# Optimization experiments

Hardware: AMD Instinct MI355X
Metric: run time of the kernel (lower is better)

## Reference

```python
import jax, jax.numpy as jnp
import numpy as np

B = 65536       # batch
F_SUB = 128     # sub-6GHz features
F_MM = 128      # mmWave features (pairs of real/imag)
H = 512         # hidden size (all three MLPs)
C = 64          # class_num (beams)
WB_SEL = 8      # number of selected wideband beams


def _mlp(x, w1, b1, w2, b2, wd, bd):
    # MLP with do_bn=False, dropout=0: Linear->ReLU->Linear->ReLU->Linear
    h = jax.nn.relu(x @ w1 + b1)
    h = jax.nn.relu(h @ w2 + b2)
    return h @ wd + bd


def setup_inputs() -> dict:
    key = jax.random.key(0)
    ks = jax.random.split(key, 16)
    w = lambda k, shape: (jax.random.normal(k, shape, jnp.float32) * 0.02)
    z = lambda n: jnp.zeros((n,), jnp.float32)
    return {
        "x": jax.random.normal(ks[0], (B, F_SUB), jnp.float32),
        "y": jax.random.normal(ks[1], (B, F_MM), jnp.float32),
        "sub_w1": w(ks[2], (F_SUB, H)), "sub_b1": z(H),
        "sub_w2": w(ks[3], (H, H)),     "sub_b2": z(H),
        "sub_wd": w(ks[4], (H, C)),     "sub_bd": z(C),
        "mm_w1": w(ks[5], (F_MM, H)),   "mm_b1": z(H),
        "mm_w2": w(ks[6], (H, H)),      "mm_b2": z(H),
        "mm_wd": w(ks[7], (H, C)),      "mm_bd": z(C),
        "att_w": w(ks[8], (2 * C, 2 * C)), "att_b": z(2 * C),
        "fus_w1": w(ks[9], (2 * C, H)), "fus_b1": z(H),
        "fus_w2": w(ks[10], (H, H)),    "fus_b2": z(H),
        "fus_wd": w(ks[11], (H, C)),    "fus_bd": z(C),
        "wb_sel": WB_SEL,
    }


def reference(x, y, sub_w1, sub_b1, sub_w2, sub_b2, sub_wd, sub_bd,
              mm_w1, mm_b1, mm_w2, mm_b2, mm_wd, mm_bd,
              att_w, att_b, fus_w1, fus_b1, fus_w2, fus_b2, fus_wd, fus_bd,
              wb_sel):
    b, f_mm = y.shape
    out_sub = _mlp(x, sub_w1, sub_b1, sub_w2, sub_b2, sub_wd, sub_bd)  # [B, C]
    class_num = out_sub.shape[1]
    wb_num = (class_num * 2) // f_mm  # int(class_num / features_mm * 2)
    # beam-group scores: sum consecutive groups of wb_num logits -> [B, f_mm/2]
    p_mm = out_sub.reshape(b, class_num // wb_num, wb_num).sum(axis=2)
    # top-k selected wideband beams (indices detached in original)
    _, idx = jax.lax.top_k(p_mm, wb_sel)               # [B, wb_sel]
    # scatter-build masked mmWave input: keep (idx*2, idx*2+1) pairs, zero rest
    rows = jnp.arange(b)[:, None]                       # [B, 1]
    mask = jnp.zeros_like(y)
    mask = mask.at[rows, idx * 2].set(1.0)
    mask = mask.at[rows, idx * 2 + 1].set(1.0)
    input_mm = y * mask
    out_mm = _mlp(input_mm, mm_w1, mm_b1, mm_w2, mm_b2, mm_wd, mm_bd)  # [B, C]
    cat = jnp.concatenate([out_sub, out_mm], axis=1)    # [B, 2C]
    out_att = jax.nn.sigmoid(cat @ att_w + att_b)       # [B, 2C]
    fused = _mlp(cat * out_att, fus_w1, fus_b1, fus_w2, fus_b2, fus_wd, fus_bd)
    return (out_sub, out_mm, fused)
```

## Files before the change

kernel.cpp:

```cpp
#include <hip/hip_runtime.h>
#include <math.h>


typedef _Float16 halfx8 __attribute__((ext_vector_type(8)));
typedef float    floatx4 __attribute__((ext_vector_type(4)));
#define MFMA16(a,b,c) __builtin_amdgcn_mfma_f32_16x16x32_f16((a),(b),(c),0,0,0)

#define BN 65536
#define MROWS 32
#define MARGIN 2e-4f

#define SM_IX0 0
#define SM_IX1 8192
#define SM_H0  16384
#define SM_H1  49152
#define SM_BYTES 81920
#define OBST 66

#define SZ_W1 65536
#define SZ_W2 262144
#define SZ_WD 32768
#define SZ_ATT 16384
#define OFF_SW1 0
#define OFF_SW2 (OFF_SW1 + SZ_W1)
#define OFF_SWD (OFF_SW2 + SZ_W2)
#define OFF_MW1 (OFF_SWD + SZ_WD)
#define OFF_MW2 (OFF_MW1 + SZ_W1)
#define OFF_MWD (OFF_MW2 + SZ_W2)
#define OFF_FW1 (OFF_MWD + SZ_WD)
#define OFF_FW2 (OFF_FW1 + SZ_W1)
#define OFF_FWD (OFF_FW2 + SZ_W2)
#define OFF_ATT (OFF_FWD + SZ_WD)

#define WS_MASKS (5u << 20)
#define WS_RROWS (6u << 20)
#define WS_RCNT  (7u << 20)
#define WS_FLAGS ((7u << 20) + 256)

enum { R_X = 0, R_Y, R_SW1, R_SB1, R_SW2, R_SB2, R_SWD, R_SBD,
       R_MW1, R_MB1, R_MW2, R_MB2, R_MWD, R_MBD, R_ATTW, R_ATTB,
       R_FW1, R_FB1, R_FW2, R_FB2, R_FWD, R_FBD, N_ROLES };

__device__ __forceinline__ float bf2f(unsigned short u) {
    return __uint_as_float((unsigned)u << 16);
}
__device__ __forceinline__ float loadf(const void* p, size_t i, int fl) {
    return fl == 1 ? bf2f(((const unsigned short*)p)[i])
         : fl == 0 ? ((const float*)p)[i] : 0.f;
}
__device__ __forceinline__ double loadd(const void* p, size_t i, int fl) {
    return fl == 1 ? (double)bf2f(((const unsigned short*)p)[i])
         : fl == 0 ? (double)((const float*)p)[i] : 0.0;
}
template<int FL>
__device__ __forceinline__ double ldw(const void* p, size_t i) {
    return FL == 1 ? (double)bf2f(((const unsigned short*)p)[i])
         : FL == 0 ? (double)((const float*)p)[i] : 0.0;
}
struct hf2 { _Float16 hi, lo; };
__device__ __forceinline__ hf2 split2h(float v) {
    hf2 r;
    r.hi = (_Float16)v;
    r.lo = (_Float16)(v - (float)r.hi);
    return r;
}
__device__ __forceinline__ int swz(int row, int colB, int rsB) {
    return (row * rsB + colB) ^ ((row & 15) << 4);
}

__device__ __forceinline__ void ld_b4(const _Float16* __restrict__ p,
                                      int base, int ktn, int kt, int l,
                                      halfx8 (&b)[4])
{
#pragma unroll
    for (int nt = 0; nt < 4; ++nt) {
        const size_t fi = ((((size_t)(base + nt)) * ktn + kt) * 64 + l) * 8;
        b[nt] = *(const halfx8*)(p + fi);
    }
}

__device__ __forceinline__ void kt_mfma(const char* __restrict__ sm,
                                        int smA0, int smA1, int rsB,
                                        int kt, int l15, int q,
                                        const halfx8 (&b)[4],
                                        floatx4 (&acc)[2][4])
{
    const int cB = kt * 64 + q * 16;
    halfx8 ahi[2], alo[2];
#pragma unroll
    for (int rt = 0; rt < 2; ++rt) {
        const int off = swz(rt * 16 + l15, cB, rsB);
        ahi[rt] = *(const halfx8*)(sm + smA0 + off);
        alo[rt] = *(const halfx8*)(sm + smA1 + off);
    }
#pragma unroll
    for (int nt = 0; nt < 4; ++nt)
#pragma unroll
        for (int rt = 0; rt < 2; ++rt) {
            acc[rt][nt] = MFMA16(alo[rt], b[nt], acc[rt][nt]);
            acc[rt][nt] = MFMA16(ahi[rt], b[nt], acc[rt][nt]);
        }
}

struct DetArgs { const void* p[N_ROLES]; int n[N_ROLES]; };

__global__ __launch_bounds__(256) void detect_kernel(DetArgs da, int* flags, int* rcnt) {
    const int role = blockIdx.x;
    if (role == 0 && threadIdx.x == 0) *rcnt = 0;
    const unsigned short* u = (const unsigned short*)da.p[role];
    int nsamp = da.n[role] / 2;
    if (nsamp > 4096) nsamp = 4096;
    __shared__ int band, nz;
    if (threadIdx.x == 0) { band = 0; nz = 0; }
    __syncthreads();
    int lb = 0, lnz = 0;
    for (int i = threadIdx.x; i < nsamp; i += 256) {
        const unsigned short v = u[2 * i];
        if (v) {
            ++lnz;
            const int e = (v >> 7) & 0xFF;
            if (e >= 100 && e <= 126) ++lb;
        }
    }
    atomicAdd(&band, lb);
    atomicAdd(&nz, lnz);
    __syncthreads();
    if (threadIdx.x == 0)
        flags[role] = (nz == 0) ? 2 : ((band * 2 > nz) ? 1 : 0);
}

struct PackArgs { const void* src[10]; int K[10], N[10], off[10], role[10]; };

__global__ __launch_bounds__(256) void pack_weights(PackArgs pa, _Float16* dst,
                                                    const int* __restrict__ flags) {
    const int m = blockIdx.y;
    const int fl = flags[pa.role[m]];
    const int K = pa.K[m], N = pa.N[m];
    const int KT = K >> 5, NT = N >> 4;
    const int total = KT * NT * 64;
    const int t = blockIdx.x * 256 + threadIdx.x;
    if (t >= total) return;
    const int l = t & 63;
    const int idx = t >> 6;
    const int kt = idx % KT;
    const int nt = idx / KT;
    const int k0 = kt * 32 + ((l >> 4) << 3);
    const int n  = nt * 16 + (l & 15);
    _Float16* dh = dst + pa.off[m] + (size_t)t * 8;
#pragma unroll
    for (int j = 0; j < 8; ++j)
        dh[j] = (_Float16)loadf(pa.src[m], (size_t)(k0 + j) * N + n, fl);
}

template <bool SUB>
__device__ __forceinline__ void mlp_core(
    char* __restrict__ sm,
    const _Float16* __restrict__ p1,
    const _Float16* __restrict__ p2,
    const _Float16* __restrict__ pd,
    const void* __restrict__ b1, int fb1,
    const void* __restrict__ b2, int fb2,
    const void* __restrict__ bd, int fbd,
    int r0, float* __restrict__ out)
{
    const int tid = threadIdx.x;
    const int l = tid & 63, w = tid >> 6, l15 = l & 15, q = l >> 4;

    floatx4 acc[2][4];
#pragma unroll
    for (int rt = 0; rt < 2; ++rt)
#pragma unroll
        for (int nt = 0; nt < 4; ++nt) acc[rt][nt] = (floatx4)0.0f;
#pragma unroll
    for (int kt = 0; kt < 4; ++kt) {
        halfx8 B[4];
        ld_b4(p1, w * 4, 4, kt, l, B);
        kt_mfma(sm, SM_IX0, SM_IX1, 256, kt, l15, q, B, acc);
    }
#pragma unroll
    for (int nt = 0; nt < 4; ++nt) {
        const int col = w * 64 + nt * 16 + l15;
        const float bias = loadf(b1, col, fb1);
#pragma unroll
        for (int rt = 0; rt < 2; ++rt)
#pragma unroll
            for (int r = 0; r < 4; ++r) {
                const int row = rt * 16 + q * 4 + r;
                float v = acc[rt][nt][r] + bias;
                v = v > 0.f ? v : 0.f;
                const hf2 s = split2h(v);
                const int o = swz(row, col * 2, 1024);
                *(_Float16*)(sm + SM_H0 + o) = s.hi;
                *(_Float16*)(sm + SM_H1 + o) = s.lo;
            }
    }
    __syncthreads();

    floatx4 acc2[2][4];
#pragma unroll
    for (int rt = 0; rt < 2; ++rt)
#pragma unroll
        for (int nt = 0; nt < 4; ++nt) acc2[rt][nt] = (floatx4)0.0f;
    for (int kt = 0; kt < 16; ++kt) {
        halfx8 B[4];
        ld_b4(p2, w * 4, 16, kt, l, B);
        kt_mfma(sm, SM_H0, SM_H1, 1024, kt, l15, q, B, acc2);
    }
    __syncthreads();
#pragma unroll
    for (int nt = 0; nt < 4; ++nt) {
        const int col = w * 64 + nt * 16 + l15;
        const float bias = loadf(b2, col, fb2);
#pragma unroll
        for (int rt = 0; rt < 2; ++rt)
#pragma unroll
            for (int r = 0; r < 4; ++r) {
                const int row = rt * 16 + q * 4 + r;
                float v = acc2[rt][nt][r] + bias;
                v = v > 0.f ? v : 0.f;
                const hf2 s = split2h(v);
                const int o = swz(row, col * 2, 1024);
                *(_Float16*)(sm + SM_H0 + o) = s.hi;
                *(_Float16*)(sm + SM_H1 + o) = s.lo;
            }
    }
    __syncthreads();

    {
        const int nt3 = w & 3, rt3 = w >> 2;
        floatx4 a3 = (floatx4)0.0f;
        for (int kt = 0; kt < 16; ++kt) {
            const size_t fi = (((size_t)(nt3 * 16 + kt)) * 64 + l) * 8;
            const halfx8 b = *(const halfx8*)(pd + fi);
            const int off = swz(rt3 * 16 + l15, kt * 64 + q * 16, 1024);
            const halfx8 ahi = *(const halfx8*)(sm + SM_H0 + off);
            const halfx8 alo = *(const halfx8*)(sm + SM_H1 + off);
            a3 = MFMA16(alo, b, a3);
            a3 = MFMA16(ahi, b, a3);
        }
        const int col = nt3 * 16 + l15;
        const float bias = loadf(bd, col, fbd);
        float* outb = (float*)sm;
#pragma unroll
        for (int r = 0; r < 4; ++r) {
            const int row = rt3 * 16 + q * 4 + r;
            const float v = a3[r] + bias;
            out[(size_t)(r0 + row) * 64 + col] = v;
            if (SUB) outb[row * OBST + col] = v;
        }
    }
    if (SUB) __syncthreads();
}

__global__ __launch_bounds__(512, 4)
void sub_mfma(const void* __restrict__ x, const _Float16* __restrict__ wpack,
              const void* __restrict__ b1, const void* __restrict__ b2,
              const void* __restrict__ bd, const int* __restrict__ flags,
              float* __restrict__ out, unsigned long long* __restrict__ masks,
              int* __restrict__ rrows, int* __restrict__ rcnt)
{
    __shared__ __align__(16) char sm[SM_BYTES];
    const int fx = flags[R_X];
    const int r0 = blockIdx.x * MROWS;

    for (int i = threadIdx.x; i < MROWS * 128; i += 512) {
        const int r = i >> 7, c = i & 127;
        const hf2 s = split2h(loadf(x, (size_t)(r0 + r) * 128 + c, fx));
        const int off = swz(r, c * 2, 256);
        *(_Float16*)(sm + SM_IX0 + off) = s.hi;
        *(_Float16*)(sm + SM_IX1 + off) = s.lo;
    }
    __syncthreads();

    mlp_core<true>(sm, wpack + OFF_SW1, wpack + OFF_SW2, wpack + OFF_SWD,
                   b1, flags[R_SB1], b2, flags[R_SB2], bd, flags[R_SBD],
                   r0, out);

    if (threadIdx.x < MROWS) {
        const float* rowp = (const float*)sm + threadIdx.x * OBST;
        float vals[9];
        int idxs[9];
#pragma unroll
        for (int j = 0; j < 9; ++j) { vals[j] = -__builtin_inff(); idxs[j] = 0; }
        for (int i = 0; i < 64; ++i) {
            const float v = rowp[i];
            if (v > vals[8]) {
                int p = 8;
                while (p > 0 && v > vals[p - 1]) {
                    vals[p] = vals[p - 1];
                    idxs[p] = idxs[p - 1];
                    --p;
                }
                vals[p] = v;
                idxs[p] = i;
            }
        }
        unsigned long long m = 0ull;
#pragma unroll
        for (int j = 0; j < 8; ++j) m |= (1ull << idxs[j]);
        masks[r0 + threadIdx.x] = m;
        if (vals[7] - vals[8] < MARGIN) {
            const int slot = atomicAdd(rcnt, 1);
            rrows[slot] = r0 + threadIdx.x;
        }
    }
}

#define RPB 16
#define OBST2 66

template<int FL, int K, int S, typename TI>
__device__ __forceinline__ void r_layer12(const void* __restrict__ W,
                                          const TI* __restrict__ in,
                                          double* __restrict__ a0,
                                          double* __restrict__ a1, int t)
{
#pragma unroll 4
    for (int k = 0; k < K; ++k) {
        const double w0 = ldw<FL>(W, (size_t)k * 512 + 2 * t);
        const double w1 = ldw<FL>(W, (size_t)k * 512 + 2 * t + 1);
#pragma unroll
        for (int r = 0; r < RPB; ++r) {
            const double xv = (double)in[r * S + k];
            a0[r] = fma(xv, w0, a0[r]);
            a1[r] = fma(xv, w1, a1[r]);
        }
    }
}

template<int FL>
__device__ __forceinline__ void r_layer3(const void* __restrict__ W,
                                         const double* __restrict__ h,
                                         int c, int rg, double* __restrict__ a)
{
#pragma unroll 4
    for (int k = 0; k < 512; ++k) {
        const double w = ldw<FL>(W, (size_t)k * 64 + c);
#pragma unroll
        for (int j = 0; j < 4; ++j)
            a[j] = fma(h[(rg * 4 + j) * 512 + k], w, a[j]);
    }
}

#define R_DISPATCH(fl, CALL)                                   \
    do {                                                       \
        if ((fl) == 1)      { CALL(1); }                       \
        else if ((fl) == 0) { CALL(0); }                       \
        else                { CALL(2); }                       \
    } while (0)

__global__ __launch_bounds__(256)
void rescue_kernel(const void* __restrict__ x,
                   const void* __restrict__ W1, const void* __restrict__ b1,
                   const void* __restrict__ W2, const void* __restrict__ b2,
                   const void* __restrict__ Wd, const void* __restrict__ bd,
                   const int* __restrict__ flags,
                   const int* __restrict__ rrows, const int* __restrict__ rcnt,
                   float* __restrict__ out, unsigned long long* __restrict__ masks)
{
    __shared__ int rowids[RPB];
    __shared__ __align__(16) char xob[RPB * OBST2 * 8];
    __shared__ __align__(16) double hsm[RPB * 512];
    float* xs = (float*)xob;
    double* ob = (double*)xob;
    const int fx = flags[R_X], f1 = flags[R_SW1], fb1 = flags[R_SB1],
              f2 = flags[R_SW2], fb2 = flags[R_SB2],
              f3 = flags[R_SWD], fb3 = flags[R_SBD];
    const int t = threadIdx.x;
    const int n = *rcnt;

    for (int g = blockIdx.x; g * RPB < n; g += gridDim.x) {
        const int base = g * RPB;
        int cnt = n - base;
        if (cnt > RPB) cnt = RPB;
        if (t < RPB) rowids[t] = rrows[base + (t < cnt ? t : cnt - 1)];
        __syncthreads();

        for (int i = t; i < RPB * 128; i += 256) {
            const int r = i >> 7, c = i & 127;
            xs[r * 128 + c] = loadf(x, (size_t)rowids[r] * 128 + c, fx);
        }
        __syncthreads();

        {
            double a0[RPB], a1[RPB];
#pragma unroll
            for (int r = 0; r < RPB; ++r) { a0[r] = 0.0; a1[r] = 0.0; }
#define L1_CALL(FL) r_layer12<FL, 128, 128, float>(W1, xs, a0, a1, t)
            R_DISPATCH(f1, L1_CALL);
#undef L1_CALL
            const double bb0 = loadd(b1, 2 * t, fb1), bb1 = loadd(b1, 2 * t + 1, fb1);
#pragma unroll
            for (int r = 0; r < RPB; ++r) {
                const double v0 = a0[r] + bb0, v1 = a1[r] + bb1;
                hsm[r * 512 + 2 * t]     = v0 > 0.0 ? v0 : 0.0;
                hsm[r * 512 + 2 * t + 1] = v1 > 0.0 ? v1 : 0.0;
            }
        }
        __syncthreads();

        {
            double a0[RPB], a1[RPB];
#pragma unroll
            for (int r = 0; r < RPB; ++r) { a0[r] = 0.0; a1[r] = 0.0; }
#define L2_CALL(FL) r_layer12<FL, 512, 512, double>(W2, hsm, a0, a1, t)
            R_DISPATCH(f2, L2_CALL);
#undef L2_CALL
            __syncthreads();
            const double bb0 = loadd(b2, 2 * t, fb2), bb1 = loadd(b2, 2 * t + 1, fb2);
#pragma unroll
            for (int r = 0; r < RPB; ++r) {
                const double v0 = a0[r] + bb0, v1 = a1[r] + bb1;
                hsm[r * 512 + 2 * t]     = v0 > 0.0 ? v0 : 0.0;
                hsm[r * 512 + 2 * t + 1] = v1 > 0.0 ? v1 : 0.0;
            }
        }
        __syncthreads();

        {
            const int c = t & 63, rg = t >> 6;
            double a[4];
#pragma unroll
            for (int j = 0; j < 4; ++j) a[j] = 0.0;
#define L3_CALL(FL) r_layer3<FL>(Wd, hsm, c, rg, a)
            R_DISPATCH(f3, L3_CALL);
#undef L3_CALL
            const double bb = loadd(bd, c, fb3);
#pragma unroll
            for (int j = 0; j < 4; ++j) {
                const int r = rg * 4 + j;
                const double v = a[j] + bb;
                ob[r * OBST2 + c] = v;
                if (r < cnt) out[(size_t)rowids[r] * 64 + c] = (float)v;
            }
        }
        __syncthreads();

        if (t < cnt) {
            double vals[8];
            int idxs[8];
#pragma unroll
            for (int j = 0; j < 8; ++j) { vals[j] = -1.0e300; idxs[j] = 0; }
            for (int i = 0; i < 64; ++i) {
                const double v = ob[t * OBST2 + i];
                if (v > vals[7]) {
                    int p = 7;
                    while (p > 0 && v > vals[p - 1]) {
                        vals[p] = vals[p - 1];
                        idxs[p] = idxs[p - 1];
                        --p;
                    }
                    vals[p] = v;
                    idxs[p] = i;
                }
            }
            unsigned long long m = 0ull;
#pragma unroll
            for (int j = 0; j < 8; ++j) m |= (1ull << idxs[j]);
            masks[rowids[t]] = m;
        }
        __syncthreads();
    }
}

__global__ __launch_bounds__(512, 4)
void mm_mfma(const unsigned long long* __restrict__ masks,
             const void* __restrict__ y, const _Float16* __restrict__ wpack,
             const void* __restrict__ b1, const void* __restrict__ b2,
             const void* __restrict__ bd, const int* __restrict__ flags,
             float* __restrict__ out)
{
    __shared__ __align__(16) char sm[SM_BYTES];
    const int fy = flags[R_Y];
    const int r0 = blockIdx.x * MROWS;

    for (int i = threadIdx.x; i < MROWS * 128; i += 512) {
        const int r = i >> 7, c = i & 127;
        const bool keep = (masks[r0 + r] >> (c >> 1)) & 1ull;
        const float v = keep ? loadf(y, (size_t)(r0 + r) * 128 + c, fy) : 0.f;
        const hf2 s = split2h(v);
        const int off = swz(r, c * 2, 256);
        *(_Float16*)(sm + SM_IX0 + off) = s.hi;
        *(_Float16*)(sm + SM_IX1 + off) = s.lo;
    }
    __syncthreads();

    mlp_core<false>(sm, wpack + OFF_MW1, wpack + OFF_MW2, wpack + OFF_MWD,
                    b1, flags[R_MB1], b2, flags[R_MB2], bd, flags[R_MBD],
                    r0, out);
}

__global__ __launch_bounds__(512, 4)
void fusion_mfma(const float* __restrict__ subf, const float* __restrict__ mmf,
                 const _Float16* __restrict__ wpack,
                 const void* __restrict__ attb,
                 const void* __restrict__ b1, const void* __restrict__ b2,
                 const void* __restrict__ bd, const int* __restrict__ flags,
                 float* __restrict__ out)
{
    __shared__ __align__(16) char sm[SM_BYTES];
    const int tid = threadIdx.x;
    const int l = tid & 63, w = tid >> 6, l15 = l & 15, q = l >> 4;
    const int r0 = blockIdx.x * MROWS;

    for (int i = tid; i < MROWS * 128; i += 512) {
        const int r = i >> 7, c = i & 127;
        const size_t row = (size_t)(r0 + r);
        const float v = (c < 64) ? subf[row * 64 + c] : mmf[row * 64 + (c - 64)];
        const hf2 s = split2h(v);
        const int off = swz(r, c * 2, 256);
        *(_Float16*)(sm + SM_IX0 + off) = s.hi;
        *(_Float16*)(sm + SM_IX1 + off) = s.lo;
    }
    __syncthreads();

    floatx4 aacc[2];
    aacc[0] = (floatx4)0.0f;
    aacc[1] = (floatx4)0.0f;
    const _Float16* patt = wpack + OFF_ATT;
#pragma unroll
    for (int kt = 0; kt < 4; ++kt) {
        const size_t fi = (((size_t)(w * 4 + kt)) * 64 + l) * 8;
        const halfx8 b = *(const halfx8*)(patt + fi);
        const int cB = kt * 64 + q * 16;
#pragma unroll
        for (int rt = 0; rt < 2; ++rt) {
            const int off = swz(rt * 16 + l15, cB, 256);
            const halfx8 ahi = *(const halfx8*)(sm + SM_IX0 + off);
            const halfx8 alo = *(const halfx8*)(sm + SM_IX1 + off);
            aacc[rt] = MFMA16(alo, b, aacc[rt]);
            aacc[rt] = MFMA16(ahi, b, aacc[rt]);
        }
    }
    const int col = w * 16 + l15;
    const float ab = loadf(attb, col, flags[R_ATTB]);
    float gated[2][4];
#pragma unroll
    for (int rt = 0; rt < 2; ++rt)
#pragma unroll
        for (int r = 0; r < 4; ++r) {
            const int rowl = rt * 16 + q * 4 + r;
            const float pre = aacc[rt][r] + ab;
            const float s = 1.f / (1.f + expf(-pre));
            const int off = swz(rowl, col * 2, 256);
            const float catv = (float)*(const _Float16*)(sm + SM_IX0 + off)
                             + (float)*(const _Float16*)(sm + SM_IX1 + off);
            gated[rt][r] = catv * s;
        }
    __syncthreads();
#pragma unroll
    for (int rt = 0; rt < 2; ++rt)
#pragma unroll
        for (int r = 0; r < 4; ++r) {
            const int rowl = rt * 16 + q * 4 + r;
            const hf2 s = split2h(gated[rt][r]);
            const int off = swz(rowl, col * 2, 256);
            *(_Float16*)(sm + SM_IX0 + off) = s.hi;
            *(_Float16*)(sm + SM_IX1 + off) = s.lo;
        }
    __syncthreads();

    mlp_core<false>(sm, wpack + OFF_FW1, wpack + OFF_FW2, wpack + OFF_FWD,
                    b1, flags[R_FB1], b2, flags[R_FB2], bd, flags[R_FBD],
                    r0, out);
}

extern "C" void kernel_launch(void* const* d_in, const int* in_sizes, int n_in,
                              void* d_out, int out_size, void* d_ws, size_t ws_size,
                              hipStream_t stream)
{
    static const int dictSizes[23] = {8388608, 8388608, 65536, 512, 262144, 512,
                                      32768, 64, 65536, 512, 262144, 512, 32768, 64,
                                      16384, 128, 65536, 512, 262144, 512, 32768, 64, 1};
    static const int dictRole[23]  = {R_X, R_Y, R_SW1, R_SB1, R_SW2, R_SB2, R_SWD, R_SBD,
                                      R_MW1, R_MB1, R_MW2, R_MB2, R_MWD, R_MBD,
                                      R_ATTW, R_ATTB, R_FW1, R_FB1, R_FW2, R_FB2,
                                      R_FWD, R_FBD, -1};
    static const int sortSizes[23] = {128, 16384, 512, 512, 64, 65536, 262144, 32768,
                                      512, 512, 64, 65536, 262144, 32768,
                                      512, 512, 64, 65536, 262144, 32768, 1,
                                      8388608, 8388608};
    static const int sortRole[23]  = {R_ATTB, R_ATTW, R_FB1, R_FB2, R_FBD, R_FW1,
                                      R_FW2, R_FWD, R_MB1, R_MB2, R_MBD, R_MW1,
                                      R_MW2, R_MWD, R_SB1, R_SB2, R_SBD, R_SW1,
                                      R_SW2, R_SWD, -1, R_X, R_Y};
    const void* rp[N_ROLES];
    int rs[N_ROLES];
    for (int i = 0; i < 23 && i < n_in; ++i)
        if (dictRole[i] >= 0) { rp[dictRole[i]] = d_in[i]; rs[dictRole[i]] = in_sizes[i]; }
    {
        bool dictOk = (n_in >= 22);
        for (int i = 0; i < 22 && dictOk; ++i)
            if (in_sizes[i] != dictSizes[i]) dictOk = false;
        if (!dictOk) {
            bool sortOk = (n_in >= 23);
            for (int i = 0; i < 23 && sortOk; ++i)
                if (in_sizes[i] != sortSizes[i]) sortOk = false;
            if (sortOk)
                for (int i = 0; i < 23; ++i)
                    if (sortRole[i] >= 0) { rp[sortRole[i]] = d_in[i]; rs[sortRole[i]] = in_sizes[i]; }
        }
    }

    _Float16* wpack = (_Float16*)d_ws;
    unsigned long long* masks = (unsigned long long*)((char*)d_ws + WS_MASKS);
    int* rrows = (int*)((char*)d_ws + WS_RROWS);
    int* rcnt  = (int*)((char*)d_ws + WS_RCNT);
    int* flags = (int*)((char*)d_ws + WS_FLAGS);

    float* out_f = (float*)d_out;
    float* sub_o = out_f;
    float* mm_o  = out_f + (size_t)BN * 64;
    float* fus_o = out_f + (size_t)2 * BN * 64;

    DetArgs da;
    for (int r = 0; r < N_ROLES; ++r) { da.p[r] = rp[r]; da.n[r] = rs[r]; }
    detect_kernel<<<N_ROLES, 256, 0, stream>>>(da, flags, rcnt);

    PackArgs pa;
    const int prole[10] = {R_SW1, R_SW2, R_SWD, R_MW1, R_MW2, R_MWD,
                           R_FW1, R_FW2, R_FWD, R_ATTW};
    const int Ks[10]   = {128, 512, 512, 128, 512, 512, 128, 512, 512, 128};
    const int Ns[10]   = {512, 512, 64, 512, 512, 64, 512, 512, 64, 128};
    const int offs[10] = {OFF_SW1, OFF_SW2, OFF_SWD, OFF_MW1, OFF_MW2,
                          OFF_MWD, OFF_FW1, OFF_FW2, OFF_FWD, OFF_ATT};
    for (int i = 0; i < 10; ++i) {
        pa.src[i] = rp[prole[i]];
        pa.K[i] = Ks[i];
        pa.N[i] = Ns[i];
        pa.off[i] = offs[i];
        pa.role[i] = prole[i];
    }
    pack_weights<<<dim3(128, 10), 256, 0, stream>>>(pa, wpack, flags);

    sub_mfma<<<BN / MROWS, 512, 0, stream>>>(
        rp[R_X], wpack, rp[R_SB1], rp[R_SB2], rp[R_SBD], flags,
        sub_o, masks, rrows, rcnt);

    rescue_kernel<<<512, 256, 0, stream>>>(
        rp[R_X], rp[R_SW1], rp[R_SB1], rp[R_SW2], rp[R_SB2], rp[R_SWD], rp[R_SBD],
        flags, rrows, rcnt, sub_o, masks);

    mm_mfma<<<BN / MROWS, 512, 0, stream>>>(
        masks, rp[R_Y], wpack, rp[R_MB1], rp[R_MB2], rp[R_MBD], flags, mm_o);

    fusion_mfma<<<BN / MROWS, 512, 0, stream>>>(
        sub_o, mm_o, wpack, rp[R_ATTB], rp[R_FB1], rp[R_FB2], rp[R_FBD],
        flags, fus_o);
}
```

Measured before the change: 809.2 us.

## Widen rescue kernel to 512 threads and transpose hidden buffer layout

The fp64 rescue kernel now uses 512 threads with one output column per thread instead of two, which halves per-thread accumulator registers and should raise occupancy. The shared hidden buffer is transposed to [k][row] so layer 2 can read row values as double2 broadcasts and layer 3 splits into 8 row groups of 2. This adds parallelism for the serial near-tie recomputation path. In exchange, each weight row is loaded by twice as many threads per block, and the launch bounds now cap registers per thread.

```diff
diff --git a/kernel.cpp b/kernel.cpp
--- a/kernel.cpp
+++ b/kernel.cpp
@@ -309,36 +309,48 @@
 #define RPB 16
 #define OBST2 66
 
-template<int FL, int K, int S, typename TI>
-__device__ __forceinline__ void r_layer12(const void* __restrict__ W,
-                                          const TI* __restrict__ in,
-                                          double* __restrict__ a0,
-                                          double* __restrict__ a1, int t)
+template<int FL>
+__device__ __forceinline__ void r1_layer(const void* __restrict__ W,
+                                         const float* __restrict__ xs,
+                                         double* __restrict__ a, int t)
 {
 #pragma unroll 4
-    for (int k = 0; k < K; ++k) {
-        const double w0 = ldw<FL>(W, (size_t)k * 512 + 2 * t);
-        const double w1 = ldw<FL>(W, (size_t)k * 512 + 2 * t + 1);
-#pragma unroll
-        for (int r = 0; r < RPB; ++r) {
-            const double xv = (double)in[r * S + k];
-            a0[r] = fma(xv, w0, a0[r]);
-            a1[r] = fma(xv, w1, a1[r]);
-        }
+    for (int k = 0; k < 128; ++k) {
+        const double w = ldw<FL>(W, (size_t)k * 512 + t);
+#pragma unroll
+        for (int r = 0; r < RPB; ++r)
+            a[r] = fma((double)xs[r * 128 + k], w, a[r]);
     }
 }
 
 template<int FL>
-__device__ __forceinline__ void r_layer3(const void* __restrict__ W,
-                                         const double* __restrict__ h,
+__device__ __forceinline__ void r2_layer(const void* __restrict__ W,
+                                         const double* __restrict__ hsm,
+                                         double* __restrict__ a, int t)
+{
+#pragma unroll 4
+    for (int k = 0; k < 512; ++k) {
+        const double w = ldw<FL>(W, (size_t)k * 512 + t);
+        const double2* hp = (const double2*)(hsm + k * 16);
+#pragma unroll
+        for (int j = 0; j < 8; ++j) {
+            const double2 hv = hp[j];
+            a[2 * j]     = fma(hv.x, w, a[2 * j]);
+            a[2 * j + 1] = fma(hv.y, w, a[2 * j + 1]);
+        }
+    }
+}
+
+template<int FL>
+__device__ __forceinline__ void r3_layer(const void* __restrict__ W,
+                                         const double* __restrict__ hsm,
                                          int c, int rg, double* __restrict__ a)
 {
 #pragma unroll 4
     for (int k = 0; k < 512; ++k) {
         const double w = ldw<FL>(W, (size_t)k * 64 + c);
-#pragma unroll
-        for (int j = 0; j < 4; ++j)
-            a[j] = fma(h[(rg * 4 + j) * 512 + k], w, a[j]);
+        a[0] = fma(hsm[k * 16 + rg * 2],     w, a[0]);
+        a[1] = fma(hsm[k * 16 + rg * 2 + 1], w, a[1]);
     }
 }
 
@@ -349,7 +361,7 @@
         else                { CALL(2); }                       \
     } while (0)
 
-__global__ __launch_bounds__(256)
+__global__ __launch_bounds__(512, 4)
 void rescue_kernel(const void* __restrict__ x,
                    const void* __restrict__ W1, const void* __restrict__ b1,
                    const void* __restrict__ W2, const void* __restrict__ b2,
@@ -360,7 +372,7 @@
 {
     __shared__ int rowids[RPB];
     __shared__ __align__(16) char xob[RPB * OBST2 * 8];
-    __shared__ __align__(16) double hsm[RPB * 512];
+    __shared__ __align__(16) double hsm[512 * RPB];
     float* xs = (float*)xob;
     double* ob = (double*)xob;
     const int fx = flags[R_X], f1 = flags[R_SW1], fb1 = flags[R_SB1],
@@ -376,59 +388,57 @@
         if (t < RPB) rowids[t] = rrows[base + (t < cnt ? t : cnt - 1)];
         __syncthreads();
 
-        for (int i = t; i < RPB * 128; i += 256) {
+        for (int i = t; i < RPB * 128; i += 512) {
             const int r = i >> 7, c = i & 127;
             xs[r * 128 + c] = loadf(x, (size_t)rowids[r] * 128 + c, fx);
         }
         __syncthreads();
 
         {
-            double a0[RPB], a1[RPB];
-#pragma unroll
-            for (int r = 0; r < RPB; ++r) { a0[r] = 0.0; a1[r] = 0.0; }
-#define L1_CALL(FL) r_layer12<FL, 128, 128, float>(W1, xs, a0, a1, t)
+            double a[RPB];
+#pragma unroll
+            for (int r = 0; r < RPB; ++r) a[r] = 0.0;
+#define L1_CALL(FL) r1_layer<FL>(W1, xs, a, t)
             R_DISPATCH(f1, L1_CALL);
 #undef L1_CALL
-            const double bb0 = loadd(b1, 2 * t, fb1), bb1 = loadd(b1, 2 * t + 1, fb1);
+            const double bb = loadd(b1, t, fb1);
 #pragma unroll
             for (int r = 0; r < RPB; ++r) {
-                const double v0 = a0[r] + bb0, v1 = a1[r] + bb1;
-                hsm[r * 512 + 2 * t]     = v0 > 0.0 ? v0 : 0.0;
-                hsm[r * 512 + 2 * t + 1] = v1 > 0.0 ? v1 : 0.0;
+                const double v = a[r] + bb;
+                hsm[t * 16 + r] = v > 0.0 ? v : 0.0;
             }
         }
         __syncthreads();
 
         {
-            double a0[RPB], a1[RPB];
-#pragma unroll
-            for (int r = 0; r < RPB; ++r) { a0[r] = 0.0; a1[r] = 0.0; }
-#define L2_CALL(FL) r_layer12<FL, 512, 512, double>(W2, hsm, a0, a1, t)
+            double a[RPB];
+#pragma unroll
+            for (int r = 0; r < RPB; ++r) a[r] = 0.0;
+#define L2_CALL(FL) r2_layer<FL>(W2, hsm, a, t)
             R_DISPATCH(f2, L2_CALL);
 #undef L2_CALL
             __syncthreads();
-            const double bb0 = loadd(b2, 2 * t, fb2), bb1 = loadd(b2, 2 * t + 1, fb2);
+            const double bb = loadd(b2, t, fb2);
 #pragma unroll
             for (int r = 0; r < RPB; ++r) {
-                const double v0 = a0[r] + bb0, v1 = a1[r] + bb1;
-                hsm[r * 512 + 2 * t]     = v0 > 0.0 ? v0 : 0.0;
-                hsm[r * 512 + 2 * t + 1] = v1 > 0.0 ? v1 : 0.0;
+                const double v = a[r] + bb;
+                hsm[t * 16 + r] = v > 0.0 ? v : 0.0;
             }
         }
         __syncthreads();
 
         {
             const int c = t & 63, rg = t >> 6;
-            double a[4];
-#pragma unroll
-            for (int j = 0; j < 4; ++j) a[j] = 0.0;
-#define L3_CALL(FL) r_layer3<FL>(Wd, hsm, c, rg, a)
+            double a[2];
+            a[0] = 0.0;
+            a[1] = 0.0;
+#define L3_CALL(FL) r3_layer<FL>(Wd, hsm, c, rg, a)
             R_DISPATCH(f3, L3_CALL);
 #undef L3_CALL
             const double bb = loadd(bd, c, fb3);
 #pragma unroll
-            for (int j = 0; j < 4; ++j) {
-                const int r = rg * 4 + j;
+            for (int j = 0; j < 2; ++j) {
+                const int r = rg * 2 + j;
                 const double v = a[j] + bb;
                 ob[r * OBST2 + c] = v;
                 if (r < cnt) out[(size_t)rowids[r] * 64 + c] = (float)v;
@@ -637,7 +647,7 @@
         rp[R_X], wpack, rp[R_SB1], rp[R_SB2], rp[R_SBD], flags,
         sub_o, masks, rrows, rcnt);
 
-    rescue_kernel<<<512, 256, 0, stream>>>(
+    rescue_kernel<<<512, 512, 0, stream>>>(
         rp[R_X], rp[R_SW1], rp[R_SB1], rp[R_SW2], rp[R_SB2], rp[R_SWD], rp[R_SBD],
         flags, rrows, rcnt, sub_o, masks);
 
```

New measurement: 956.1 us. 18.2% more time.
